# Performance work log

Measured on AMD Instinct MI355X. Metric: run time of the kernel, lower is better.

The kernel has to match this reference:

```python
import jax, jax.numpy as jnp
import numpy as np

# Problem constants (from config / init_kwargs)
B = 32768          # batch_size
T = 20             # T_observation
N = 4              # N_agents
D = 8              # state_dim
H = 64             # gru_hidden_size


def setup_inputs() -> dict:
    key = jax.random.key(0)
    ks = jax.random.split(key, 6)
    s = lambda fan_in: 1.0 / np.sqrt(fan_in)
    return {
        "x": jax.random.normal(ks[0], (B, T * N * D), dtype=jnp.float32),
        # per-agent GRU weights: input proj (no bias), hidden proj (with bias); 3H = r|z|n
        "Wi": jax.random.normal(ks[1], (N, D, 3 * H), dtype=jnp.float32) * s(D),
        "Wh": jax.random.normal(ks[2], (N, H, 3 * H), dtype=jnp.float32) * s(H),
        "bh": jnp.zeros((N, 3 * H), dtype=jnp.float32),
        # MLP head: 256 -> 256 -> 128 -> 8
        "W0": jax.random.normal(ks[3], (N * H, 256), dtype=jnp.float32) * s(N * H),
        "b0": jnp.zeros((256,), dtype=jnp.float32),
        "W1": jax.random.normal(ks[4], (256, 128), dtype=jnp.float32) * s(256),
        "b1": jnp.zeros((128,), dtype=jnp.float32),
        "Wout": jax.random.normal(ks[5], (128, 8), dtype=jnp.float32) * s(128),
        "bout": jnp.zeros((8,), dtype=jnp.float32),
    }


def reference(x, Wi, Wh, bh, W0, b0, W1, b1, Wout, bout):
    b = x.shape[0]
    xr = x.reshape(b, T, N, D)
    # Precompute input-side gate projections for all agents/timesteps at once.
    xi = jnp.einsum("btnd,ndk->tbnk", xr, Wi)  # [T, B, N, 3H]

    def step(h, xi_t):
        # h: [B, N, H]; xi_t: [B, N, 3H]
        hg = jnp.einsum("bnh,nhk->bnk", h, Wh) + bh  # [B, N, 3H]
        ir, iz, inn = jnp.split(xi_t, 3, axis=-1)
        hr, hz, hn = jnp.split(hg, 3, axis=-1)
        r = jax.nn.sigmoid(ir + hr)
        z = jax.nn.sigmoid(iz + hz)
        n = jnp.tanh(inn + r * hn)
        h_new = (1.0 - z) * n + z * h  # flax GRUCell update
        return h_new, None

    h0 = jnp.zeros((b, N, H), dtype=x.dtype)
    hT, _ = jax.lax.scan(step, h0, xi)
    feat = hT.reshape(b, N * H)  # concat per-agent final hidden states

    h1 = jax.nn.relu(feat @ W0 + b0)
    h2 = jax.nn.relu(h1 @ W1 + b1)  # dropout deterministic -> identity
    goals = h2 @ Wout + bout
    return goals
```

## Files before the change

### kernel.cpp

```cpp
#include <hip/hip_runtime.h>
#include <math.h>

#define BT 32768
#define TT 20
#define NA 4
#define DD 8
#define HH 64

typedef short short8 __attribute__((ext_vector_type(8)));
typedef float f32x4 __attribute__((ext_vector_type(4)));
typedef unsigned short ushort;
typedef unsigned int uint;

#define SC1 -1.4426950408889634f
#define SC2 -2.8853900817779268f

__device__ __forceinline__ void bsplit(float v, ushort& h, ushort& l) {
    uint u = __float_as_uint(v);
    uint hu = u & 0xFFFF0000u;
    h = (ushort)(hu >> 16);
    float r = v - __uint_as_float(hu);
    l = (ushort)(__float_as_uint(r) >> 16);
}

__global__ void prep_gruA(const float* __restrict__ Wh, const float* __restrict__ Wi,
                          const float* __restrict__ bh, uint4* __restrict__ AG) {
    int gid = blockIdx.x * 256 + threadIdx.x;
    int l = gid & 63;
    int r2 = gid >> 6;
    int fid = r2 % 20;
    int jt = (r2 / 20) & 3;
    int n = r2 / 80;
    int s = fid & 1;
    int gk = fid >> 1;
    int g, kq;
    if (gk < 9) { g = gk / 3; kq = gk % 3; } else { g = 3; kq = 2; }
    int j = jt * 16 + (l & 15);
    int lk = (l >> 4) & 3;
    float scale = (g < 2) ? SC1 : SC2;

    uint wds[4];
    for (int i = 0; i < 4; ++i) {
        uint pk = 0;
        for (int half = 0; half < 2; ++half) {
            int e = 2 * i + half;
            int k = kq * 32 + 8 * lk + e;
            float v = 0.f;
            if (g < 3) {
                if (k < 64)            v = Wh[(size_t)(n * 64 + k) * 192 + g * 64 + j];
                else if (k < 72) { if (g < 2) v = Wi[(size_t)(n * 8 + (k - 64)) * 192 + g * 64 + j]; }
                else if (k == 72)      v = bh[n * 192 + g * 64 + j];
            } else {
                if (k >= 64 && k < 72) v = Wi[(size_t)(n * 8 + (k - 64)) * 192 + 128 + j];
            }
            v *= scale;
            ushort hi, lo; bsplit(v, hi, lo);
            ushort b = s ? lo : hi;
            pk |= ((uint)b) << (16 * half);
        }
        wds[i] = pk;
    }
    uint4 u; u.x = wds[0]; u.y = wds[1]; u.z = wds[2]; u.w = wds[3];
    AG[gid] = u;
}

__global__ void prep_mlpW(const float* __restrict__ W, uint4* __restrict__ dst,
                          int NT, int NKQ, int Nreal) {
    int gid = blockIdx.x * 256 + threadIdx.x;
    if (gid >= NT * NKQ * 2 * 64) return;
    int l = gid & 63;
    int s = (gid >> 6) & 1;
    int rr = gid >> 7;
    int kq = rr % NKQ;
    int nt = rr / NKQ;
    int o = nt * 16 + (l & 15);
    int lk = (l >> 4) & 3;
    uint wds[4];
    for (int i = 0; i < 4; ++i) {
        uint pk = 0;
        for (int half = 0; half < 2; ++half) {
            int e = 2 * i + half;
            int k = kq * 32 + 8 * lk + e;
            float v = (o < Nreal) ? W[(size_t)k * Nreal + o] : 0.f;
            ushort hi, lo; bsplit(v, hi, lo);
            ushort b = s ? lo : hi;
            pk |= ((uint)b) << (16 * half);
        }
        wds[i] = pk;
    }
    uint4 u; u.x = wds[0]; u.y = wds[1]; u.z = wds[2]; u.w = wds[3];
    dst[gid] = u;
}

#define LDK 88
#define PLANE (32 * LDK + 32)

__global__ __launch_bounds__(256, 3)
void gru_kernel(const float* __restrict__ x, const uint4* __restrict__ AG,
                ushort* __restrict__ featH, ushort* __restrict__ featL) {
    __shared__ __align__(16) ushort Bs[2][2][PLANE];
    const int tid = threadIdx.x;
    const int l = tid & 63;
    const int w = tid >> 6;
    const int lrow = l & 15;
    const int lk = l >> 4;
    const int n = blockIdx.y;
    const int bg = blockIdx.x * 32;

    {
        uint4 z = {0, 0, 0, 0};
        uint4* p = (uint4*)&Bs[0][0][0];
        for (int i = tid; i < (int)(sizeof(Bs) / 16); i += 256) p[i] = z;
    }
    __syncthreads();

    short8 A[20];
    const uint4* ab = AG + (size_t)(n * 4 + w) * 1280 + l;
#pragma unroll
    for (int f = 0; f < 20; ++f) {
        uint4 v = ab[f * 64];
        A[f] = *(short8*)&v;
    }

    const int m0 = tid >> 3, d0 = tid & 7;
    const float* __restrict__ xp = x + (size_t)(bg + m0) * 640 + n * 8 + d0;

    {
        float v = xp[0];
        ushort hi, lo; bsplit(v, hi, lo);
        Bs[0][0][m0 * LDK + 64 + d0] = hi;
        Bs[0][1][m0 * LDK + 64 + d0] = lo;
    }
    if (tid < 64) {
        int m = tid & 31, bu = tid >> 5;
        Bs[bu][0][m * LDK + 72] = 0x3F80;
    }
    __syncthreads();

    f32x4 hold[2];
#pragma unroll
    for (int nt = 0; nt < 2; ++nt)
#pragma unroll
        for (int r = 0; r < 4; ++r) hold[nt][r] = 0.f;

    for (int t = 0; t < TT; ++t) {
        const int p = t & 1;
        float xnext = (t < 19) ? xp[(t + 1) * 32] : 0.f;

        const ushort* __restrict__ BH = &Bs[p][0][0];
        const ushort* __restrict__ BL = &Bs[p][1][0];
        ushort* __restrict__ WH = &Bs[p ^ 1][0][0];
        ushort* __restrict__ WL = &Bs[p ^ 1][1][0];

        f32x4 acc[2][4];
#pragma unroll
        for (int nt = 0; nt < 2; ++nt)
#pragma unroll
            for (int g = 0; g < 4; ++g)
#pragma unroll
                for (int r = 0; r < 4; ++r) acc[nt][g][r] = 0.f;

#pragma unroll
        for (int nt = 0; nt < 2; ++nt) {
#pragma unroll
            for (int kq = 0; kq < 3; ++kq) {
                const int boff = (nt * 16 + lrow) * LDK + kq * 32 + 8 * lk;
                short8 bhf = *(const short8*)&BH[boff];
                short8 blf = *(const short8*)&BL[boff];
#pragma unroll
                for (int g = 0; g < 3; ++g) {
                    acc[nt][g] = __builtin_amdgcn_mfma_f32_16x16x32_bf16(A[(g * 3 + kq) * 2 + 0], bhf, acc[nt][g], 0, 0, 0);
                    acc[nt][g] = __builtin_amdgcn_mfma_f32_16x16x32_bf16(A[(g * 3 + kq) * 2 + 1], bhf, acc[nt][g], 0, 0, 0);
                    acc[nt][g] = __builtin_amdgcn_mfma_f32_16x16x32_bf16(A[(g * 3 + kq) * 2 + 0], blf, acc[nt][g], 0, 0, 0);
                }
                if (kq == 2) {
                    acc[nt][3] = __builtin_amdgcn_mfma_f32_16x16x32_bf16(A[18], bhf, acc[nt][3], 0, 0, 0);
                    acc[nt][3] = __builtin_amdgcn_mfma_f32_16x16x32_bf16(A[19], bhf, acc[nt][3], 0, 0, 0);
                    acc[nt][3] = __builtin_amdgcn_mfma_f32_16x16x32_bf16(A[18], blf, acc[nt][3], 0, 0, 0);
                }
            }
        }

#pragma unroll
        for (int nt = 0; nt < 2; ++nt) {
            ushort hh[4], hl[4];
#pragma unroll
            for (int r = 0; r < 4; ++r) {
                float rg = __builtin_amdgcn_rcpf(1.f + __builtin_amdgcn_exp2f(acc[nt][0][r]));
                float zg = __builtin_amdgcn_rcpf(1.f + __builtin_amdgcn_exp2f(acc[nt][1][r]));
                float sarg = fmaf(rg, acc[nt][2][r], acc[nt][3][r]);
                float sg = __builtin_amdgcn_rcpf(1.f + __builtin_amdgcn_exp2f(sarg));
                float ng = fmaf(2.f, sg, -1.f);
                float hv = fmaf(zg, hold[nt][r] - ng, ng);
                hold[nt][r] = hv;
                bsplit(hv, hh[r], hl[r]);
            }
            const int wboff = (nt * 16 + lrow) * LDK + w * 16 + 4 * lk;
            uint2 ph, pl;
            ph.x = (uint)hh[0] | ((uint)hh[1] << 16);
            ph.y = (uint)hh[2] | ((uint)hh[3] << 16);
            pl.x = (uint)hl[0] | ((uint)hl[1] << 16);
            pl.y = (uint)hl[2] | ((uint)hl[3] << 16);
            *(uint2*)&WH[wboff] = ph;
            *(uint2*)&WL[wboff] = pl;
        }
        if (t < 19) {
            ushort hi, lo; bsplit(xnext, hi, lo);
            WH[m0 * LDK + 64 + d0] = hi;
            WL[m0 * LDK + 64 + d0] = lo;
        }
        __syncthreads();
    }

#pragma unroll
    for (int nt = 0; nt < 2; ++nt) {
        ushort fh[4], fl[4];
#pragma unroll
        for (int r = 0; r < 4; ++r) bsplit(hold[nt][r], fh[r], fl[r]);
        uint2 ph, pl;
        ph.x = (uint)fh[0] | ((uint)fh[1] << 16);
        ph.y = (uint)fh[2] | ((uint)fh[3] << 16);
        pl.x = (uint)fl[0] | ((uint)fl[1] << 16);
        pl.y = (uint)fl[2] | ((uint)fl[3] << 16);
        size_t fo = (size_t)(bg + nt * 16 + lrow) * 256 + n * 64 + w * 16 + 4 * lk;
        *(uint2*)&featH[fo] = ph;
        *(uint2*)&featL[fo] = pl;
    }
}

__global__ __launch_bounds__(256, 3)
void mlp_kernel(const ushort* __restrict__ featH, const ushort* __restrict__ featL,
                const uint4* __restrict__ W0F, const uint4* __restrict__ W1F,
                const uint4* __restrict__ W2F, const float* __restrict__ b0,
                const float* __restrict__ b1, const float* __restrict__ bout,
                float* __restrict__ out) {
    __shared__ __align__(16) ushort s1[2][32][264];
    __shared__ __align__(16) ushort s2[2][32][136];
    const int tid = threadIdx.x;
    const int l = tid & 63;
    const int w = tid >> 6;
    const int lrow = l & 15;
    const int lk = l >> 4;
    const int bg = blockIdx.x * 32;

    f32x4 a0[2][4];
#pragma unroll
    for (int bt = 0; bt < 2; ++bt)
#pragma unroll
        for (int q = 0; q < 4; ++q)
#pragma unroll
            for (int r = 0; r < 4; ++r) a0[bt][q][r] = 0.f;

    for (int kq = 0; kq < 8; ++kq) {
        short8 aH[2], aL[2];
#pragma unroll
        for (int bt = 0; bt < 2; ++bt) {
            size_t off = (size_t)(bg + bt * 16 + lrow) * 256 + kq * 32 + 8 * lk;
            aH[bt] = *(const short8*)&featH[off];
            aL[bt] = *(const short8*)&featL[off];
        }
#pragma unroll
        for (int q = 0; q < 4; ++q) {
            int nt = w * 4 + q;
            short8 bH = *(const short8*)&W0F[((nt * 8 + kq) * 2 + 0) * 64 + l];
            short8 bL = *(const short8*)&W0F[((nt * 8 + kq) * 2 + 1) * 64 + l];
#pragma unroll
            for (int bt = 0; bt < 2; ++bt) {
                a0[bt][q] = __builtin_amdgcn_mfma_f32_16x16x32_bf16(aH[bt], bH, a0[bt][q], 0, 0, 0);
                a0[bt][q] = __builtin_amdgcn_mfma_f32_16x16x32_bf16(aL[bt], bH, a0[bt][q], 0, 0, 0);
                a0[bt][q] = __builtin_amdgcn_mfma_f32_16x16x32_bf16(aH[bt], bL, a0[bt][q], 0, 0, 0);
            }
        }
    }
#pragma unroll
    for (int bt = 0; bt < 2; ++bt)
#pragma unroll
        for (int q = 0; q < 4; ++q) {
            int nn = (w * 4 + q) * 16 + lrow;
            float bias = b0[nn];
            int row0 = bt * 16 + 4 * lk;
#pragma unroll
            for (int r = 0; r < 4; ++r) {
                float v = a0[bt][q][r] + bias;
                v = v > 0.f ? v : 0.f;
                ushort hi, lo; bsplit(v, hi, lo);
                s1[0][row0 + r][nn] = hi;
                s1[1][row0 + r][nn] = lo;
            }
        }
    __syncthreads();

    f32x4 a1[2][2];
#pragma unroll
    for (int bt = 0; bt < 2; ++bt)
#pragma unroll
        for (int u = 0; u < 2; ++u)
#pragma unroll
            for (int r = 0; r < 4; ++r) a1[bt][u][r] = 0.f;

    for (int kq = 0; kq < 8; ++kq) {
        short8 aH[2], aL[2];
#pragma unroll
        for (int bt = 0; bt < 2; ++bt) {
            aH[bt] = *(const short8*)&s1[0][bt * 16 + lrow][kq * 32 + 8 * lk];
            aL[bt] = *(const short8*)&s1[1][bt * 16 + lrow][kq * 32 + 8 * lk];
        }
#pragma unroll
        for (int u = 0; u < 2; ++u) {
            int nt1 = w + 4 * u;
            short8 bH = *(const short8*)&W1F[((nt1 * 8 + kq) * 2 + 0) * 64 + l];
            short8 bL = *(const short8*)&W1F[((nt1 * 8 + kq) * 2 + 1) * 64 + l];
#pragma unroll
            for (int bt = 0; bt < 2; ++bt) {
                a1[bt][u] = __builtin_amdgcn_mfma_f32_16x16x32_bf16(aH[bt], bH, a1[bt][u], 0, 0, 0);
                a1[bt][u] = __builtin_amdgcn_mfma_f32_16x16x32_bf16(aL[bt], bH, a1[bt][u], 0, 0, 0);
                a1[bt][u] = __builtin_amdgcn_mfma_f32_16x16x32_bf16(aH[bt], bL, a1[bt][u], 0, 0, 0);
            }
        }
    }
#pragma unroll
    for (int bt = 0; bt < 2; ++bt)
#pragma unroll
        for (int u = 0; u < 2; ++u) {
            int nn = (w + 4 * u) * 16 + lrow;
            float bias = b1[nn];
            int row0 = bt * 16 + 4 * lk;
#pragma unroll
            for (int r = 0; r < 4; ++r) {
                float v = a1[bt][u][r] + bias;
                v = v > 0.f ? v : 0.f;
                ushort hi, lo; bsplit(v, hi, lo);
                s2[0][row0 + r][nn] = hi;
                s2[1][row0 + r][nn] = lo;
            }
        }
    __syncthreads();

    if (w < 2) {
        const int bt = w;
        f32x4 a2;
#pragma unroll
        for (int r = 0; r < 4; ++r) a2[r] = 0.f;
        for (int kq = 0; kq < 4; ++kq) {
            short8 aH = *(const short8*)&s2[0][bt * 16 + lrow][kq * 32 + 8 * lk];
            short8 aL = *(const short8*)&s2[1][bt * 16 + lrow][kq * 32 + 8 * lk];
            short8 bH = *(const short8*)&W2F[(kq * 2 + 0) * 64 + l];
            short8 bL = *(const short8*)&W2F[(kq * 2 + 1) * 64 + l];
            a2 = __builtin_amdgcn_mfma_f32_16x16x32_bf16(aH, bH, a2, 0, 0, 0);
            a2 = __builtin_amdgcn_mfma_f32_16x16x32_bf16(aL, bH, a2, 0, 0, 0);
            a2 = __builtin_amdgcn_mfma_f32_16x16x32_bf16(aH, bL, a2, 0, 0, 0);
        }
        if (lrow < 8) {
            float bo = bout[lrow];
#pragma unroll
            for (int r = 0; r < 4; ++r)
                out[(size_t)(bg + bt * 16 + 4 * lk + r) * 8 + lrow] = a2[r] + bo;
        }
    }
}

extern "C" void kernel_launch(void* const* d_in, const int* in_sizes, int n_in,
                              void* d_out, int out_size, void* d_ws, size_t ws_size,
                              hipStream_t stream) {
    const float* x    = (const float*)d_in[0];
    const float* Wi   = (const float*)d_in[1];
    const float* Wh   = (const float*)d_in[2];
    const float* bh   = (const float*)d_in[3];
    const float* W0   = (const float*)d_in[4];
    const float* b0   = (const float*)d_in[5];
    const float* W1   = (const float*)d_in[6];
    const float* b1   = (const float*)d_in[7];
    const float* Wout = (const float*)d_in[8];
    const float* bout = (const float*)d_in[9];

    char* wsb = (char*)d_ws;
    ushort* featH = (ushort*)wsb;
    ushort* featL = (ushort*)(wsb + 16777216);
    uint4* AG  = (uint4*)(wsb + 33554432);
    uint4* W0F = (uint4*)(wsb + 33554432 + 327680);
    uint4* W1F = (uint4*)(wsb + 33554432 + 327680 + 262144);
    uint4* W2F = (uint4*)(wsb + 33554432 + 327680 + 262144 + 131072);

    prep_gruA<<<80, 256, 0, stream>>>(Wh, Wi, bh, AG);
    prep_mlpW<<<64, 256, 0, stream>>>(W0, W0F, 16, 8, 256);
    prep_mlpW<<<32, 256, 0, stream>>>(W1, W1F, 8, 8, 128);
    prep_mlpW<<<2, 256, 0, stream>>>(Wout, W2F, 1, 4, 8);
    gru_kernel<<<dim3(BT / 32, NA), 256, 0, stream>>>(x, AG, featH, featL);
    mlp_kernel<<<BT / 32, 256, 0, stream>>>(featH, featL, W0F, W1F, W2F, b0, b1, bout, (float*)d_out);
}
```

Before: 380.8 us.

## Switch split-precision MFMAs to fp16, restructure GRU waves and swizzle LDS

Replaces the bf16 hi/lo split with an fp16 hi/lo split throughout. In the MLP the weights become a single fp16 term, cutting MFMAs per tile from three to two. The GRU kernel now has each wave cover two hidden tiles for one batch tile, so B-fragment LDS reads are shared, but it holds twice the A registers with occupancy lowered to 2. LDS padding is replaced by XOR swizzles, the four prep kernels are merged into one launch, and the final-step hidden write to LDS is skipped. fp16 has a narrower exponent range than bf16, so values outside it could overflow or lose accuracy, and dropping the low weight term reduces MLP precision.

```diff
diff --git a/kernel.cpp b/kernel.cpp
--- a/kernel.cpp
+++ b/kernel.cpp
@@ -7,7 +7,7 @@
 #define DD 8
 #define HH 64
 
-typedef short short8 __attribute__((ext_vector_type(8)));
+typedef _Float16 half8 __attribute__((ext_vector_type(8)));
 typedef float f32x4 __attribute__((ext_vector_type(4)));
 typedef unsigned short ushort;
 typedef unsigned int uint;
@@ -15,111 +15,119 @@
 #define SC1 -1.4426950408889634f
 #define SC2 -2.8853900817779268f
 
-__device__ __forceinline__ void bsplit(float v, ushort& h, ushort& l) {
-    uint u = __float_as_uint(v);
-    uint hu = u & 0xFFFF0000u;
-    h = (ushort)(hu >> 16);
-    float r = v - __uint_as_float(hu);
-    l = (ushort)(__float_as_uint(r) >> 16);
-}
-
-__global__ void prep_gruA(const float* __restrict__ Wh, const float* __restrict__ Wi,
-                          const float* __restrict__ bh, uint4* __restrict__ AG) {
-    int gid = blockIdx.x * 256 + threadIdx.x;
-    int l = gid & 63;
-    int r2 = gid >> 6;
-    int fid = r2 % 20;
-    int jt = (r2 / 20) & 3;
-    int n = r2 / 80;
-    int s = fid & 1;
-    int gk = fid >> 1;
-    int g, kq;
-    if (gk < 9) { g = gk / 3; kq = gk % 3; } else { g = 3; kq = 2; }
-    int j = jt * 16 + (l & 15);
-    int lk = (l >> 4) & 3;
-    float scale = (g < 2) ? SC1 : SC2;
-
-    uint wds[4];
-    for (int i = 0; i < 4; ++i) {
-        uint pk = 0;
-        for (int half = 0; half < 2; ++half) {
-            int e = 2 * i + half;
-            int k = kq * 32 + 8 * lk + e;
-            float v = 0.f;
-            if (g < 3) {
-                if (k < 64)            v = Wh[(size_t)(n * 64 + k) * 192 + g * 64 + j];
-                else if (k < 72) { if (g < 2) v = Wi[(size_t)(n * 8 + (k - 64)) * 192 + g * 64 + j]; }
-                else if (k == 72)      v = bh[n * 192 + g * 64 + j];
-            } else {
-                if (k >= 64 && k < 72) v = Wi[(size_t)(n * 8 + (k - 64)) * 192 + 128 + j];
-            }
-            v *= scale;
-            ushort hi, lo; bsplit(v, hi, lo);
-            ushort b = s ? lo : hi;
-            pk |= ((uint)b) << (16 * half);
-        }
-        wds[i] = pk;
-    }
-    uint4 u; u.x = wds[0]; u.y = wds[1]; u.z = wds[2]; u.w = wds[3];
-    AG[gid] = u;
-}
-
-__global__ void prep_mlpW(const float* __restrict__ W, uint4* __restrict__ dst,
-                          int NT, int NKQ, int Nreal) {
-    int gid = blockIdx.x * 256 + threadIdx.x;
-    if (gid >= NT * NKQ * 2 * 64) return;
-    int l = gid & 63;
-    int s = (gid >> 6) & 1;
-    int rr = gid >> 7;
-    int kq = rr % NKQ;
-    int nt = rr / NKQ;
-    int o = nt * 16 + (l & 15);
-    int lk = (l >> 4) & 3;
-    uint wds[4];
-    for (int i = 0; i < 4; ++i) {
-        uint pk = 0;
-        for (int half = 0; half < 2; ++half) {
-            int e = 2 * i + half;
-            int k = kq * 32 + 8 * lk + e;
-            float v = (o < Nreal) ? W[(size_t)k * Nreal + o] : 0.f;
-            ushort hi, lo; bsplit(v, hi, lo);
-            ushort b = s ? lo : hi;
-            pk |= ((uint)b) << (16 * half);
-        }
-        wds[i] = pk;
-    }
-    uint4 u; u.x = wds[0]; u.y = wds[1]; u.z = wds[2]; u.w = wds[3];
-    dst[gid] = u;
-}
-
-#define LDK 88
-#define PLANE (32 * LDK + 32)
-
-__global__ __launch_bounds__(256, 3)
+__device__ __forceinline__ ushort f16b(float v) {
+    _Float16 h = (_Float16)v;
+    return *(ushort*)&h;
+}
+__device__ __forceinline__ void fsplit(float v, ushort& hi, ushort& lo) {
+    _Float16 h = (_Float16)v;
+    hi = *(ushort*)&h;
+    float r = v - (float)h;
+    _Float16 lw = (_Float16)r;
+    lo = *(ushort*)&lw;
+}
+
+__global__ void prep_all(const float* __restrict__ Wh, const float* __restrict__ Wi,
+                         const float* __restrict__ bh, const float* __restrict__ W0,
+                         const float* __restrict__ W1, const float* __restrict__ Wout,
+                         uint4* __restrict__ AG, uint4* __restrict__ W0F,
+                         uint4* __restrict__ W1F, uint4* __restrict__ W2F) {
+    const int gid = blockIdx.x * 256 + threadIdx.x;
+    if (gid < 20480) {
+        const int l = gid & 63;
+        const int r2 = gid >> 6;
+        const int fid = r2 % 20;
+        const int jt = (r2 / 20) & 3;
+        const int n = r2 / 80;
+        const int s = fid & 1;
+        const int gk = fid >> 1;
+        int g, kq;
+        if (gk < 9) { g = gk / 3; kq = gk % 3; } else { g = 3; kq = 2; }
+        const int j = jt * 16 + (l & 15);
+        const int lk = (l >> 4) & 3;
+        const float scale = (g < 2) ? SC1 : SC2;
+        uint wds[4];
+        for (int i = 0; i < 4; ++i) {
+            uint pk = 0;
+            for (int hf = 0; hf < 2; ++hf) {
+                const int e = 2 * i + hf;
+                const int k = kq * 32 + 8 * lk + e;
+                float v = 0.f;
+                if (g < 3) {
+                    if (k < 64)       v = Wh[(size_t)(n * 64 + k) * 192 + g * 64 + j];
+                    else if (k < 72)  { if (g < 2) v = Wi[(size_t)(n * 8 + (k - 64)) * 192 + g * 64 + j]; }
+                    else if (k == 72) v = bh[n * 192 + g * 64 + j];
+                } else {
+                    if (k >= 64 && k < 72) v = Wi[(size_t)(n * 8 + (k - 64)) * 192 + 128 + j];
+                }
+                v *= scale;
+                ushort hi, lo; fsplit(v, hi, lo);
+                pk |= ((uint)(s ? lo : hi)) << (16 * hf);
+            }
+            wds[i] = pk;
+        }
+        uint4 u; u.x = wds[0]; u.y = wds[1]; u.z = wds[2]; u.w = wds[3];
+        AG[gid] = u;
+    } else if (gid < 33024) {
+        int id; const float* W; uint4* dst; int Nreal;
+        if (gid < 28672)      { id = gid - 20480; W = W0;   dst = W0F; Nreal = 256; }
+        else if (gid < 32768) { id = gid - 28672; W = W1;   dst = W1F; Nreal = 128; }
+        else                  { id = gid - 32768; W = Wout; dst = W2F; Nreal = 8;   }
+        const int l = id & 63;
+        const int rr = id >> 6;
+        const int kq = rr & 7;
+        const int nt = rr >> 3;
+        const int o = nt * 16 + (l & 15);
+        const int lk = (l >> 4) & 3;
+        const int ocols = (Nreal < 16) ? Nreal : ((Nreal + 15) & ~15);
+        uint wds[4];
+        for (int i = 0; i < 4; ++i) {
+            uint pk = 0;
+            for (int hf = 0; hf < 2; ++hf) {
+                const int e = 2 * i + hf;
+                const int k = kq * 32 + 8 * lk + e;
+                float v = 0.f;
+                if (o < Nreal) v = W[(size_t)k * Nreal + o];
+                pk |= ((uint)f16b(v)) << (16 * hf);
+            }
+            wds[i] = pk;
+        }
+        uint4 u; u.x = wds[0]; u.y = wds[1]; u.z = wds[2]; u.w = wds[3];
+        dst[id] = u;
+        (void)ocols;
+    }
+}
+
+__global__ __launch_bounds__(256, 2)
 void gru_kernel(const float* __restrict__ x, const uint4* __restrict__ AG,
                 ushort* __restrict__ featH, ushort* __restrict__ featL) {
-    __shared__ __align__(16) ushort Bs[2][2][PLANE];
+    __shared__ __align__(16) ushort Bs[2][2][32 * 128];
     const int tid = threadIdx.x;
     const int l = tid & 63;
     const int w = tid >> 6;
     const int lrow = l & 15;
     const int lk = l >> 4;
+    const int jt2 = w >> 1;
+    const int nt = w & 1;
     const int n = blockIdx.y;
     const int bg = blockIdx.x * 32;
 
     {
         uint4 z = {0, 0, 0, 0};
         uint4* p = (uint4*)&Bs[0][0][0];
-        for (int i = tid; i < (int)(sizeof(Bs) / 16); i += 256) p[i] = z;
+        for (int i = tid; i < 2048; i += 256) p[i] = z;
     }
     __syncthreads();
 
-    short8 A[20];
-    const uint4* ab = AG + (size_t)(n * 4 + w) * 1280 + l;
-#pragma unroll
-    for (int f = 0; f < 20; ++f) {
-        uint4 v = ab[f * 64];
-        A[f] = *(short8*)&v;
+    half8 A[2][20];
+#pragma unroll
+    for (int jl = 0; jl < 2; ++jl) {
+        const uint4* __restrict__ ab = AG + (size_t)((n * 4 + (jt2 * 2 + jl)) * 20) * 64 + l;
+#pragma unroll
+        for (int f = 0; f < 20; ++f) {
+            uint4 v = ab[f * 64];
+            A[jl][f] = *(half8*)&v;
+        }
     }
 
     const int m0 = tid >> 3, d0 = tid & 7;
@@ -127,25 +135,30 @@
 
     {
         float v = xp[0];
-        ushort hi, lo; bsplit(v, hi, lo);
-        Bs[0][0][m0 * LDK + 64 + d0] = hi;
-        Bs[0][1][m0 * LDK + 64 + d0] = lo;
+        ushort hi, lo; fsplit(v, hi, lo);
+        const int gsw = 8 ^ (m0 & 7);
+        Bs[0][0][m0 * 128 + gsw * 8 + d0] = hi;
+        Bs[0][1][m0 * 128 + gsw * 8 + d0] = lo;
     }
     if (tid < 64) {
-        int m = tid & 31, bu = tid >> 5;
-        Bs[bu][0][m * LDK + 72] = 0x3F80;
+        const int m = tid & 31, bu = tid >> 5;
+        Bs[bu][0][m * 128 + (9 ^ (m & 7)) * 8 + 0] = 0x3C00;
     }
     __syncthreads();
 
     f32x4 hold[2];
 #pragma unroll
-    for (int nt = 0; nt < 2; ++nt)
-#pragma unroll
-        for (int r = 0; r < 4; ++r) hold[nt][r] = 0.f;
+    for (int jl = 0; jl < 2; ++jl)
+#pragma unroll
+        for (int r = 0; r < 4; ++r) hold[jl][r] = 0.f;
+
+    const int rbase = (nt * 16 + lrow) * 128;
+    const int key = lrow & 7;
 
     for (int t = 0; t < TT; ++t) {
         const int p = t & 1;
-        float xnext = (t < 19) ? xp[(t + 1) * 32] : 0.f;
+        float xnext = 0.f;
+        if (t < TT - 1) xnext = xp[(t + 1) * 32];
 
         const ushort* __restrict__ BH = &Bs[p][0][0];
         const ushort* __restrict__ BL = &Bs[p][1][0];
@@ -154,75 +167,82 @@
 
         f32x4 acc[2][4];
 #pragma unroll
-        for (int nt = 0; nt < 2; ++nt)
+        for (int jl = 0; jl < 2; ++jl)
 #pragma unroll
             for (int g = 0; g < 4; ++g)
 #pragma unroll
-                for (int r = 0; r < 4; ++r) acc[nt][g][r] = 0.f;
-
-#pragma unroll
-        for (int nt = 0; nt < 2; ++nt) {
-#pragma unroll
-            for (int kq = 0; kq < 3; ++kq) {
-                const int boff = (nt * 16 + lrow) * LDK + kq * 32 + 8 * lk;
-                short8 bhf = *(const short8*)&BH[boff];
-                short8 blf = *(const short8*)&BL[boff];
+                for (int r = 0; r < 4; ++r) acc[jl][g][r] = 0.f;
+
+#pragma unroll
+        for (int kq = 0; kq < 3; ++kq) {
+            const int gsw = (kq * 4 + lk) ^ key;
+            const half8 bhf = *(const half8*)&BH[rbase + gsw * 8];
+            const half8 blf = *(const half8*)&BL[rbase + gsw * 8];
+#pragma unroll
+            for (int jl = 0; jl < 2; ++jl) {
 #pragma unroll
                 for (int g = 0; g < 3; ++g) {
-                    acc[nt][g] = __builtin_amdgcn_mfma_f32_16x16x32_bf16(A[(g * 3 + kq) * 2 + 0], bhf, acc[nt][g], 0, 0, 0);
-                    acc[nt][g] = __builtin_amdgcn_mfma_f32_16x16x32_bf16(A[(g * 3 + kq) * 2 + 1], bhf, acc[nt][g], 0, 0, 0);
-                    acc[nt][g] = __builtin_amdgcn_mfma_f32_16x16x32_bf16(A[(g * 3 + kq) * 2 + 0], blf, acc[nt][g], 0, 0, 0);
+                    acc[jl][g] = __builtin_amdgcn_mfma_f32_16x16x32_f16(A[jl][(g * 3 + kq) * 2 + 0], bhf, acc[jl][g], 0, 0, 0);
+                    acc[jl][g] = __builtin_amdgcn_mfma_f32_16x16x32_f16(A[jl][(g * 3 + kq) * 2 + 1], bhf, acc[jl][g], 0, 0, 0);
+                    acc[jl][g] = __builtin_amdgcn_mfma_f32_16x16x32_f16(A[jl][(g * 3 + kq) * 2 + 0], blf, acc[jl][g], 0, 0, 0);
                 }
                 if (kq == 2) {
-                    acc[nt][3] = __builtin_amdgcn_mfma_f32_16x16x32_bf16(A[18], bhf, acc[nt][3], 0, 0, 0);
-                    acc[nt][3] = __builtin_amdgcn_mfma_f32_16x16x32_bf16(A[19], bhf, acc[nt][3], 0, 0, 0);
-                    acc[nt][3] = __builtin_amdgcn_mfma_f32_16x16x32_bf16(A[18], blf, acc[nt][3], 0, 0, 0);
+                    acc[jl][3] = __builtin_amdgcn_mfma_f32_16x16x32_f16(A[jl][18], bhf, acc[jl][3], 0, 0, 0);
+                    acc[jl][3] = __builtin_amdgcn_mfma_f32_16x16x32_f16(A[jl][19], bhf, acc[jl][3], 0, 0, 0);
+                    acc[jl][3] = __builtin_amdgcn_mfma_f32_16x16x32_f16(A[jl][18], blf, acc[jl][3], 0, 0, 0);
                 }
             }
         }
 
 #pragma unroll
-        for (int nt = 0; nt < 2; ++nt) {
-            ushort hh[4], hl[4];
+        for (int jl = 0; jl < 2; ++jl) {
+            float hv[4];
 #pragma unroll
             for (int r = 0; r < 4; ++r) {
-                float rg = __builtin_amdgcn_rcpf(1.f + __builtin_amdgcn_exp2f(acc[nt][0][r]));
-                float zg = __builtin_amdgcn_rcpf(1.f + __builtin_amdgcn_exp2f(acc[nt][1][r]));
-                float sarg = fmaf(rg, acc[nt][2][r], acc[nt][3][r]);
-                float sg = __builtin_amdgcn_rcpf(1.f + __builtin_amdgcn_exp2f(sarg));
-                float ng = fmaf(2.f, sg, -1.f);
-                float hv = fmaf(zg, hold[nt][r] - ng, ng);
-                hold[nt][r] = hv;
-                bsplit(hv, hh[r], hl[r]);
-            }
-            const int wboff = (nt * 16 + lrow) * LDK + w * 16 + 4 * lk;
-            uint2 ph, pl;
-            ph.x = (uint)hh[0] | ((uint)hh[1] << 16);
-            ph.y = (uint)hh[2] | ((uint)hh[3] << 16);
-            pl.x = (uint)hl[0] | ((uint)hl[1] << 16);
-            pl.y = (uint)hl[2] | ((uint)hl[3] << 16);
-            *(uint2*)&WH[wboff] = ph;
-            *(uint2*)&WL[wboff] = pl;
-        }
-        if (t < 19) {
-            ushort hi, lo; bsplit(xnext, hi, lo);
-            WH[m0 * LDK + 64 + d0] = hi;
-            WL[m0 * LDK + 64 + d0] = lo;
+                const float rg = __builtin_amdgcn_rcpf(1.f + __builtin_amdgcn_exp2f(acc[jl][0][r]));
+                const float zg = __builtin_amdgcn_rcpf(1.f + __builtin_amdgcn_exp2f(acc[jl][1][r]));
+                const float sarg = fmaf(rg, acc[jl][2][r], acc[jl][3][r]);
+                const float sg = __builtin_amdgcn_rcpf(1.f + __builtin_amdgcn_exp2f(sarg));
+                const float ng = fmaf(2.f, sg, -1.f);
+                hv[r] = fmaf(zg, hold[jl][r] - ng, ng);
+                hold[jl][r] = hv[r];
+            }
+            if (t < TT - 1) {
+                ushort hh[4], hl[4];
+#pragma unroll
+                for (int r = 0; r < 4; ++r) fsplit(hv[r], hh[r], hl[r]);
+                const int jtg = jt2 * 2 + jl;
+                const int gsw = (2 * jtg + (lk >> 1)) ^ key;
+                const int off = rbase + gsw * 8 + 4 * (lk & 1);
+                uint2 ph, pl;
+                ph.x = (uint)hh[0] | ((uint)hh[1] << 16);
+                ph.y = (uint)hh[2] | ((uint)hh[3] << 16);
+                pl.x = (uint)hl[0] | ((uint)hl[1] << 16);
+                pl.y = (uint)hl[2] | ((uint)hl[3] << 16);
+                *(uint2*)&WH[off] = ph;
+                *(uint2*)&WL[off] = pl;
+            }
+        }
+        if (t < TT - 1) {
+            ushort hi, lo; fsplit(xnext, hi, lo);
+            const int gsw = 8 ^ (m0 & 7);
+            WH[m0 * 128 + gsw * 8 + d0] = hi;
+            WL[m0 * 128 + gsw * 8 + d0] = lo;
         }
         __syncthreads();
     }
 
 #pragma unroll
-    for (int nt = 0; nt < 2; ++nt) {
+    for (int jl = 0; jl < 2; ++jl) {
         ushort fh[4], fl[4];
 #pragma unroll
-        for (int r = 0; r < 4; ++r) bsplit(hold[nt][r], fh[r], fl[r]);
+        for (int r = 0; r < 4; ++r) fsplit(hold[jl][r], fh[r], fl[r]);
         uint2 ph, pl;
         ph.x = (uint)fh[0] | ((uint)fh[1] << 16);
         ph.y = (uint)fh[2] | ((uint)fh[3] << 16);
         pl.x = (uint)fl[0] | ((uint)fl[1] << 16);
         pl.y = (uint)fl[2] | ((uint)fl[3] << 16);
-        size_t fo = (size_t)(bg + nt * 16 + lrow) * 256 + n * 64 + w * 16 + 4 * lk;
+        const size_t fo = (size_t)(bg + nt * 16 + lrow) * 256 + n * 64 + (jt2 * 2 + jl) * 16 + 4 * lk;
         *(uint2*)&featH[fo] = ph;
         *(uint2*)&featL[fo] = pl;
     }
@@ -234,8 +254,8 @@
                 const uint4* __restrict__ W2F, const float* __restrict__ b0,
                 const float* __restrict__ b1, const float* __restrict__ bout,
                 float* __restrict__ out) {
-    __shared__ __align__(16) ushort s1[2][32][264];
-    __shared__ __align__(16) ushort s2[2][32][136];
+    __shared__ __align__(16) ushort s1[2][32 * 256];
+    __shared__ __align__(16) ushort s2[2][32 * 128];
     const int tid = threadIdx.x;
     const int l = tid & 63;
     const int w = tid >> 6;
@@ -251,24 +271,23 @@
 #pragma unroll
             for (int r = 0; r < 4; ++r) a0[bt][q][r] = 0.f;
 
+#pragma unroll 2
     for (int kq = 0; kq < 8; ++kq) {
-        short8 aH[2], aL[2];
+        half8 aH[2], aL[2];
 #pragma unroll
         for (int bt = 0; bt < 2; ++bt) {
-            size_t off = (size_t)(bg + bt * 16 + lrow) * 256 + kq * 32 + 8 * lk;
-            aH[bt] = *(const short8*)&featH[off];
-            aL[bt] = *(const short8*)&featL[off];
+            const size_t off = (size_t)(bg + bt * 16 + lrow) * 256 + kq * 32 + 8 * lk;
+            aH[bt] = *(const half8*)&featH[off];
+            aL[bt] = *(const half8*)&featL[off];
         }
 #pragma unroll
         for (int q = 0; q < 4; ++q) {
-            int nt = w * 4 + q;
-            short8 bH = *(const short8*)&W0F[((nt * 8 + kq) * 2 + 0) * 64 + l];
-            short8 bL = *(const short8*)&W0F[((nt * 8 + kq) * 2 + 1) * 64 + l];
+            const uint4 bv = W0F[((w * 4 + q) * 8 + kq) * 64 + l];
+            const half8 bw = *(const half8*)&bv;
 #pragma unroll
             for (int bt = 0; bt < 2; ++bt) {
-                a0[bt][q] = __builtin_amdgcn_mfma_f32_16x16x32_bf16(aH[bt], bH, a0[bt][q], 0, 0, 0);
-                a0[bt][q] = __builtin_amdgcn_mfma_f32_16x16x32_bf16(aL[bt], bH, a0[bt][q], 0, 0, 0);
-                a0[bt][q] = __builtin_amdgcn_mfma_f32_16x16x32_bf16(aH[bt], bL, a0[bt][q], 0, 0, 0);
+                a0[bt][q] = __builtin_amdgcn_mfma_f32_16x16x32_f16(aH[bt], bw, a0[bt][q], 0, 0, 0);
+                a0[bt][q] = __builtin_amdgcn_mfma_f32_16x16x32_f16(aL[bt], bw, a0[bt][q], 0, 0, 0);
             }
         }
     }
@@ -276,16 +295,18 @@
     for (int bt = 0; bt < 2; ++bt)
 #pragma unroll
         for (int q = 0; q < 4; ++q) {
-            int nn = (w * 4 + q) * 16 + lrow;
-            float bias = b0[nn];
-            int row0 = bt * 16 + 4 * lk;
+            const int nn = (w * 4 + q) * 16 + lrow;
+            const float bias = b0[nn];
+            const int gc = nn >> 3, sub = nn & 7;
 #pragma unroll
             for (int r = 0; r < 4; ++r) {
+                const int row = bt * 16 + 4 * lk + r;
                 float v = a0[bt][q][r] + bias;
                 v = v > 0.f ? v : 0.f;
-                ushort hi, lo; bsplit(v, hi, lo);
-                s1[0][row0 + r][nn] = hi;
-                s1[1][row0 + r][nn] = lo;
+                ushort hi, lo; fsplit(v, hi, lo);
+                const int gsw = gc ^ (row & 7);
+                s1[0][row * 256 + gsw * 8 + sub] = hi;
+                s1[1][row * 256 + gsw * 8 + sub] = lo;
             }
         }
     __syncthreads();
@@ -298,23 +319,24 @@
 #pragma unroll
             for (int r = 0; r < 4; ++r) a1[bt][u][r] = 0.f;
 
+#pragma unroll 2
     for (int kq = 0; kq < 8; ++kq) {
-        short8 aH[2], aL[2];
+        half8 aH[2], aL[2];
 #pragma unroll
         for (int bt = 0; bt < 2; ++bt) {
-            aH[bt] = *(const short8*)&s1[0][bt * 16 + lrow][kq * 32 + 8 * lk];
-            aL[bt] = *(const short8*)&s1[1][bt * 16 + lrow][kq * 32 + 8 * lk];
+            const int row = bt * 16 + lrow;
+            const int gsw = (kq * 4 + lk) ^ (row & 7);
+            aH[bt] = *(const half8*)&s1[0][row * 256 + gsw * 8];
+            aL[bt] = *(const half8*)&s1[1][row * 256 + gsw * 8];
         }
 #pragma unroll
         for (int u = 0; u < 2; ++u) {
-            int nt1 = w + 4 * u;
-            short8 bH = *(const short8*)&W1F[((nt1 * 8 + kq) * 2 + 0) * 64 + l];
-            short8 bL = *(const short8*)&W1F[((nt1 * 8 + kq) * 2 + 1) * 64 + l];
+            const uint4 bv = W1F[((w + 4 * u) * 8 + kq) * 64 + l];
+            const half8 bw = *(const half8*)&bv;
 #pragma unroll
             for (int bt = 0; bt < 2; ++bt) {
-                a1[bt][u] = __builtin_amdgcn_mfma_f32_16x16x32_bf16(aH[bt], bH, a1[bt][u], 0, 0, 0);
-                a1[bt][u] = __builtin_amdgcn_mfma_f32_16x16x32_bf16(aL[bt], bH, a1[bt][u], 0, 0, 0);
-                a1[bt][u] = __builtin_amdgcn_mfma_f32_16x16x32_bf16(aH[bt], bL, a1[bt][u], 0, 0, 0);
+                a1[bt][u] = __builtin_amdgcn_mfma_f32_16x16x32_f16(aH[bt], bw, a1[bt][u], 0, 0, 0);
+                a1[bt][u] = __builtin_amdgcn_mfma_f32_16x16x32_f16(aL[bt], bw, a1[bt][u], 0, 0, 0);
             }
         }
     }
@@ -322,16 +344,18 @@
     for (int bt = 0; bt < 2; ++bt)
 #pragma unroll
         for (int u = 0; u < 2; ++u) {
-            int nn = (w + 4 * u) * 16 + lrow;
-            float bias = b1[nn];
-            int row0 = bt * 16 + 4 * lk;
+            const int nn = (w + 4 * u) * 16 + lrow;
+            const float bias = b1[nn];
+            const int gc = nn >> 3, sub = nn & 7;
 #pragma unroll
             for (int r = 0; r < 4; ++r) {
+                const int row = bt * 16 + 4 * lk + r;
                 float v = a1[bt][u][r] + bias;
                 v = v > 0.f ? v : 0.f;
-                ushort hi, lo; bsplit(v, hi, lo);
-                s2[0][row0 + r][nn] = hi;
-                s2[1][row0 + r][nn] = lo;
+                ushort hi, lo; fsplit(v, hi, lo);
+                const int gsw = gc ^ (row & 7);
+                s2[0][row * 128 + gsw * 8 + sub] = hi;
+                s2[1][row * 128 + gsw * 8 + sub] = lo;
             }
         }
     __syncthreads();
@@ -341,17 +365,19 @@
         f32x4 a2;
 #pragma unroll
         for (int r = 0; r < 4; ++r) a2[r] = 0.f;
+#pragma unroll
         for (int kq = 0; kq < 4; ++kq) {
-            short8 aH = *(const short8*)&s2[0][bt * 16 + lrow][kq * 32 + 8 * lk];
-            short8 aL = *(const short8*)&s2[1][bt * 16 + lrow][kq * 32 + 8 * lk];
-            short8 bH = *(const short8*)&W2F[(kq * 2 + 0) * 64 + l];
-            short8 bL = *(const short8*)&W2F[(kq * 2 + 1) * 64 + l];
-            a2 = __builtin_amdgcn_mfma_f32_16x16x32_bf16(aH, bH, a2, 0, 0, 0);
-            a2 = __builtin_amdgcn_mfma_f32_16x16x32_bf16(aL, bH, a2, 0, 0, 0);
-            a2 = __builtin_amdgcn_mfma_f32_16x16x32_bf16(aH, bL, a2, 0, 0, 0);
+            const int row = bt * 16 + lrow;
+            const int gsw = (kq * 4 + lk) ^ (row & 7);
+            const half8 aH = *(const half8*)&s2[0][row * 128 + gsw * 8];
+            const half8 aL = *(const half8*)&s2[1][row * 128 + gsw * 8];
+            const uint4 bv = W2F[kq * 64 + l];
+            const half8 bw = *(const half8*)&bv;
+            a2 = __builtin_amdgcn_mfma_f32_16x16x32_f16(aH, bw, a2, 0, 0, 0);
+            a2 = __builtin_amdgcn_mfma_f32_16x16x32_f16(aL, bw, a2, 0, 0, 0);
         }
         if (lrow < 8) {
-            float bo = bout[lrow];
+            const float bo = bout[lrow];
 #pragma unroll
             for (int r = 0; r < 4; ++r)
                 out[(size_t)(bg + bt * 16 + 4 * lk + r) * 8 + lrow] = a2[r] + bo;
@@ -378,13 +404,10 @@
     ushort* featL = (ushort*)(wsb + 16777216);
     uint4* AG  = (uint4*)(wsb + 33554432);
     uint4* W0F = (uint4*)(wsb + 33554432 + 327680);
-    uint4* W1F = (uint4*)(wsb + 33554432 + 327680 + 262144);
-    uint4* W2F = (uint4*)(wsb + 33554432 + 327680 + 262144 + 131072);
-
-    prep_gruA<<<80, 256, 0, stream>>>(Wh, Wi, bh, AG);
-    prep_mlpW<<<64, 256, 0, stream>>>(W0, W0F, 16, 8, 256);
-    prep_mlpW<<<32, 256, 0, stream>>>(W1, W1F, 8, 8, 128);
-    prep_mlpW<<<2, 256, 0, stream>>>(Wout, W2F, 1, 4, 8);
+    uint4* W1F = (uint4*)(wsb + 33554432 + 327680 + 131072);
+    uint4* W2F = (uint4*)(wsb + 33554432 + 327680 + 131072 + 65536);
+
+    prep_all<<<129, 256, 0, stream>>>(Wh, Wi, bh, W0, W1, Wout, AG, W0F, W1F, W2F);
     gru_kernel<<<dim3(BT / 32, NA), 256, 0, stream>>>(x, AG, featH, featL);
     mlp_kernel<<<BT / 32, 256, 0, stream>>>(featH, featL, W0F, W1F, W2F, b0, b1, bout, (float*)d_out);
 }
```

Result: no change. 378.6 us (-0.6%).
